# Performance work log

Measured on AMD Instinct MI355X. Metric: run time of the kernel, lower is better.

The kernel has to match this reference:

```python
import jax, jax.numpy as jnp
import numpy as np

C = 256
CQK = C // 8  # 32

def setup_inputs() -> dict:
    key = jax.random.key(0)
    ks = jax.random.split(key, 9)
    B, H, W = 4, 64, 64
    shp = (B, C, H, W)
    v = jax.random.normal(ks[0], shp, dtype=jnp.float32)
    k = jax.random.normal(ks[1], shp, dtype=jnp.float32)
    q = jax.random.normal(ks[2], shp, dtype=jnp.float32)
    s = 1.0 / np.sqrt(C)
    Wq = jax.random.normal(ks[3], (CQK, C), dtype=jnp.float32) * s
    bq = jnp.zeros((CQK,), dtype=jnp.float32)
    Wk = jax.random.normal(ks[4], (CQK, C), dtype=jnp.float32) * s
    bk = jnp.zeros((CQK,), dtype=jnp.float32)
    Wv = jax.random.normal(ks[5], (C, C), dtype=jnp.float32) * s
    bv = jnp.zeros((C,), dtype=jnp.float32)
    # torch inits gamma=0 (out == v); use small nonzero so attention path is exercised
    gamma = jnp.full((1,), 0.5, dtype=jnp.float32)
    return {"v": v, "k": k, "q": q, "Wq": Wq, "bq": bq, "Wk": Wk, "bk": bk,
            "Wv": Wv, "bv": bv, "gamma": gamma}

def reference(v, k, q, Wq, bq, Wk, bk, Wv, bv, gamma):
    B, Cc, Hh, Ww = v.shape
    N = Hh * Ww
    # 1x1 convs == per-pixel channel matmuls
    pq = jnp.einsum('oc,bchw->bohw', Wq, q) + bq[None, :, None, None]  # B,CQK,H,W
    pk = jnp.einsum('oc,bchw->bohw', Wk, k) + bk[None, :, None, None]
    pv = jnp.einsum('oc,bchw->bohw', Wv, v) + bv[None, :, None, None]  # B,C,H,W
    pq = pq.reshape(B, -1, N)  # B,d,N
    pk = pk.reshape(B, -1, N)
    pv = pv.reshape(B, Cc, N)
    # energy[b,n,m] = <q_n, k_m>; softmax over m (keys)
    energy = jnp.einsum('bdn,bdm->bnm', pq, pk)
    attn = jax.nn.softmax(energy, axis=-1)
    # out[b,c,n] = sum_m v[b,c,m] * attn[b,n,m]
    out = jnp.einsum('bcm,bnm->bcn', pv, attn).reshape(B, Cc, Hh, Ww)
    return gamma * out + v
```

## Files before the change

### kernel.cpp

```cpp
#include <hip/hip_runtime.h>
#include <hip/hip_bf16.h>

typedef __attribute__((ext_vector_type(8))) short short8_t;
typedef __attribute__((ext_vector_type(4))) unsigned short ushort4_t;
typedef __attribute__((ext_vector_type(4))) float float4_t;

#define B_   4
#define C_   256
#define N_   4096
#define DQK  32
#define LOG2E 1.4426950408889634f

#define VMCNT4   asm volatile("s_waitcnt vmcnt(4)" ::: "memory")
#define VMCNT0   asm volatile("s_waitcnt vmcnt(0)" ::: "memory")
#define LGKM0    asm volatile("s_waitcnt lgkmcnt(0)" ::: "memory")
#define SBAR     __builtin_amdgcn_s_barrier()
#define SCHEDB   __builtin_amdgcn_sched_barrier(0)

__device__ __forceinline__ unsigned short f2bf(float x) {
    union { float f; unsigned int u; } v; v.f = x;
    unsigned int r = v.u + 0x7FFFu + ((v.u >> 16) & 1u);
    return (unsigned short)(r >> 16);
}
__device__ __forceinline__ unsigned short f2bf_hw(float x) {
    return __bfloat16_as_ushort(__float2bfloat16(x));
}
__device__ __forceinline__ float bf2f(unsigned short u) {
    union { unsigned int u; float f; } v; v.u = ((unsigned int)u) << 16; return v.f;
}

__global__ __launch_bounds__(256) void cast_w_k(
        const float* __restrict__ Wq, const float* __restrict__ Wk,
        const float* __restrict__ Wv,
        unsigned short* __restrict__ Wqb, unsigned short* __restrict__ Wkb,
        unsigned short* __restrict__ Wvb) {
    int i = blockIdx.x * 256 + threadIdx.x;
    if (i < 8192)            Wqb[i] = f2bf(Wq[i]);
    else if (i < 16384)      Wkb[i - 8192] = f2bf(Wk[i - 8192]);
    else                     Wvb[i - 16384] = f2bf(Wv[i - 16384]);
}

__global__ __launch_bounds__(256) void proj_qk_k(
        const float* __restrict__ q_in, const float* __restrict__ k_in,
        const unsigned short* __restrict__ Wqb, const unsigned short* __restrict__ Wkb,
        const float* __restrict__ bq, const float* __restrict__ bk,
        unsigned short* __restrict__ pqT, unsigned short* __restrict__ pkT) {
    int b = blockIdx.y, z = blockIdx.z;
    const float* X = z ? k_in : q_in;
    const unsigned short* W = z ? Wkb : Wqb;
    const float* bias = z ? bk : bq;
    unsigned short* P = z ? pkT : pqT;
    float scl = z ? 1.0f : LOG2E;
    int tid = threadIdx.x, wave = tid >> 6, lane = tid & 63, l15 = lane & 15, g = lane >> 4;
    int nb = blockIdx.x * 64 + wave * 16;
    float4_t acc0 = {0.f, 0.f, 0.f, 0.f}, acc1 = {0.f, 0.f, 0.f, 0.f};
    const float* Xcol = X + (size_t)b * C_ * N_ + nb + l15;
#pragma unroll
    for (int kk = 0; kk < 8; ++kk) {
        short8_t a;
#pragma unroll
        for (int j = 0; j < 8; ++j)
            a[j] = (short)f2bf(Xcol[(size_t)(kk * 32 + 8 * g + j) * N_]);
        short8_t b0 = *(const short8_t*)(W + (size_t)l15 * C_ + kk * 32 + 8 * g);
        short8_t b1 = *(const short8_t*)(W + (size_t)(16 + l15) * C_ + kk * 32 + 8 * g);
        acc0 = __builtin_amdgcn_mfma_f32_16x16x32_bf16(a, b0, acc0, 0, 0, 0);
        acc1 = __builtin_amdgcn_mfma_f32_16x16x32_bf16(a, b1, acc1, 0, 0, 0);
    }
#pragma unroll
    for (int r = 0; r < 4; ++r) {
        int n = nb + 4 * g + r;
        P[((size_t)b * N_ + n) * DQK + l15]      = f2bf((acc0[r] + bias[l15]) * scl);
        P[((size_t)b * N_ + n) * DQK + 16 + l15] = f2bf((acc1[r] + bias[16 + l15]) * scl);
    }
}

__global__ __launch_bounds__(256) void proj_v_k(
        const float* __restrict__ v_in, const unsigned short* __restrict__ Wvb,
        const float* __restrict__ bv, unsigned short* __restrict__ pv) {
    int b = blockIdx.y;
    int tid = threadIdx.x, wave = tid >> 6, lane = tid & 63, l15 = lane & 15, g = lane >> 4;
    int mb = blockIdx.x * 16;
    int m = mb + l15;
    int k32 = m & 31;
    int pcol = (k32 < 16) ? ((k32 >> 2) * 8 + (k32 & 3))
                          : (((k32 - 16) >> 2) * 8 + 4 + (k32 & 3));
    int mcol = (m & ~31) + pcol;
    float4_t acc[4];
#pragma unroll
    for (int i = 0; i < 4; ++i) acc[i] = (float4_t){0.f, 0.f, 0.f, 0.f};
    const float* Vcol = v_in + (size_t)b * C_ * N_ + mb + l15;
#pragma unroll
    for (int kk = 0; kk < 8; ++kk) {
        short8_t bf;
#pragma unroll
        for (int j = 0; j < 8; ++j)
            bf[j] = (short)f2bf(Vcol[(size_t)(kk * 32 + 8 * g + j) * N_]);
#pragma unroll
        for (int ct = 0; ct < 4; ++ct) {
            short8_t af = *(const short8_t*)(Wvb + (size_t)(wave * 64 + ct * 16 + l15) * C_ + kk * 32 + 8 * g);
            acc[ct] = __builtin_amdgcn_mfma_f32_16x16x32_bf16(af, bf, acc[ct], 0, 0, 0);
        }
    }
#pragma unroll
    for (int ct = 0; ct < 4; ++ct)
#pragma unroll
        for (int r = 0; r < 4; ++r) {
            int c = wave * 64 + ct * 16 + 4 * g + r;
            pv[((size_t)b * C_ + c) * N_ + mcol] = f2bf(acc[ct][r] + bv[c]);
        }
}

__global__ __launch_bounds__(512, 4) void attn_split_k(
        const unsigned short* __restrict__ pqT, const unsigned short* __restrict__ pkT,
        const unsigned short* __restrict__ pv,
        unsigned short* __restrict__ accP, float* __restrict__ lP, int KS) {
    __shared__ __align__(16) unsigned short VT[256][64];
    __shared__ __align__(16) short8_t Pl[2][4][2][4][16];
    int nqb = gridDim.x;
    int lin = blockIdx.x + nqb * (blockIdx.y + KS * blockIdx.z);
    int cpx = (nqb * KS * 4) >> 3;
    int sl  = (lin & 7) * cpx + (lin >> 3);
    int qbi = sl % nqb;
    int s   = (sl / nqb) % KS;
    int b   = sl / (nqb * KS);

    int kps = N_ / KS, ks0 = s * kps, nt = kps >> 6;
    int tid = threadIdx.x, wave = tid >> 6, lane = tid & 63, l15 = lane & 15, g = lane >> 4;
    int qb = qbi * 64;
    bool prod = wave < 4;
    int qs = wave & 3;
    int rl = lane >> 3, cl = (lane & 7) ^ rl;
    int sw = (l15 & 7) << 4;

    short8_t qf = *(const short8_t*)(pqT + ((size_t)b * N_ + qb + qs * 16 + l15) * DQK + 8 * g);
    float4_t acc[2][4];
#pragma unroll
    for (int i = 0; i < 2; ++i)
#pragma unroll
        for (int j = 0; j < 4; ++j) acc[i][j] = (float4_t){0.f, 0.f, 0.f, 0.f};
    float l_acc = 0.f;
    const float4_t zero4 = {0.f, 0.f, 0.f, 0.f};
    const char* pvb8 = (const char*)(pv + (size_t)b * C_ * N_);
    const char* pkTb = (const char*)pkT + (size_t)b * N_ * DQK * 2;

    unsigned soff[4];
#pragma unroll
    for (int i = 0; i < 4; ++i)
        soff[i] = (unsigned)(((wave * 32 + i * 8 + rl) * N_ + ks0 + 8 * cl) * 2);
    unsigned koff = (unsigned)(((ks0 + l15) * DQK + 8 * g) * 2);
    const char* vbA = (const char*)&VT[0][0] + (wave * 32 + l15) * 128 + ((16 * g) ^ sw);
    const char* vbB = (const char*)&VT[0][0] + (wave * 32 + l15) * 128 + ((64 + 16 * g) ^ sw);
    char* PlB = (char*)&Pl[0][0][0][0][0];
    const char* prd = PlB + g * 256 + l15 * 16;
    char* pwr = PlB + qs * 2048 + g * 256 + l15 * 16;

    short8_t kf[4];

#define STAGE()                                                               \
    _Pragma("unroll")                                                         \
    for (int i_ = 0; i_ < 4; ++i_) {                                          \
        __builtin_amdgcn_global_load_lds(                                     \
            (const __attribute__((address_space(1))) unsigned int*)(const void*)(pvb8 + soff[i_]), \
            (__attribute__((address_space(3))) unsigned int*)(void*)((char*)&VT[0][0] + (wave * 32 + i_ * 8) * 128), \
            16, 0, 0);                                                        \
        soff[i_] += 128;                                                      \
    }

#define KFLOAD()                                                              \
    _Pragma("unroll")                                                         \
    for (int it_ = 0; it_ < 4; ++it_)                                         \
        kf[it_] = *(const short8_t*)(pkTb + koff + it_ * 1024);               \
    koff += 4096;

#define VREAD(DST)                                                            \
    _Pragma("unroll")                                                         \
    for (int ct_ = 0; ct_ < 2; ++ct_) {                                       \
        DST[ct_][0] = *(const short8_t*)(vbA + ct_ * 2048);                   \
        DST[ct_][1] = *(const short8_t*)(vbB + ct_ * 2048);                   \
    }

#define PFREAD(DST, CBOFF)                                                    \
    _Pragma("unroll")                                                         \
    for (int qt_ = 0; qt_ < 4; ++qt_)                                         \
        _Pragma("unroll")                                                     \
        for (int kh_ = 0; kh_ < 2; ++kh_)                                     \
            DST[qt_][kh_] = *(const short8_t*)(prd + (CBOFF) + qt_ * 2048 + kh_ * 1024);

#define QKWR(NBOFF)                                                           \
    {                                                                          \
        float4_t sv_[4];                                                       \
        _Pragma("unroll")                                                      \
        for (int it_ = 0; it_ < 4; ++it_)                                      \
            sv_[it_] = __builtin_amdgcn_mfma_f32_16x16x32_bf16(kf[it_], qf, zero4, 0, 0, 0); \
        float p_[16];                                                          \
        _Pragma("unroll")                                                      \
        for (int it_ = 0; it_ < 4; ++it_)                                      \
            _Pragma("unroll")                                                  \
            for (int r_ = 0; r_ < 4; ++r_)                                     \
                p_[it_ * 4 + r_] = exp2f(sv_[it_][r_]);                        \
        l_acc += ((p_[0] + p_[1]) + (p_[2] + p_[3])) + ((p_[4] + p_[5]) + (p_[6] + p_[7])) \
               + ((p_[8] + p_[9]) + (p_[10] + p_[11])) + ((p_[12] + p_[13]) + (p_[14] + p_[15])); \
        short8_t pb0_, pb1_;                                                   \
        _Pragma("unroll")                                                      \
        for (int j_ = 0; j_ < 4; ++j_) {                                       \
            pb0_[j_]     = (short)f2bf_hw(p_[j_]);                             \
            pb0_[4 + j_] = (short)f2bf_hw(p_[4 + j_]);                         \
            pb1_[j_]     = (short)f2bf_hw(p_[8 + j_]);                         \
            pb1_[4 + j_] = (short)f2bf_hw(p_[12 + j_]);                        \
        }                                                                      \
        *(short8_t*)(pwr + (NBOFF))        = pb0_;                             \
        *(short8_t*)(pwr + (NBOFF) + 1024) = pb1_;                             \
    }

#define PVM(VF, PF)                                                           \
    _Pragma("unroll")                                                         \
    for (int ct_ = 0; ct_ < 2; ++ct_)                                         \
        _Pragma("unroll")                                                     \
        for (int qt_ = 0; qt_ < 4; ++qt_) {                                   \
            acc[ct_][qt_] = __builtin_amdgcn_mfma_f32_16x16x32_bf16(VF[ct_][0], PF[qt_][0], acc[ct_][qt_], 0, 0, 0); \
            acc[ct_][qt_] = __builtin_amdgcn_mfma_f32_16x16x32_bf16(VF[ct_][1], PF[qt_][1], acc[ct_][qt_], 0, 0, 0); \
        }

#define BODY(T, CBOFF, NBOFF)                                                 \
    {                                                                          \
        if (prod) { VMCNT4; } else { VMCNT0; }                                 \
        SCHEDB;                                                                \
        short8_t vf_[2][2], pf_[4][2];                                         \
        VREAD(vf_)                                                             \
        PFREAD(pf_, CBOFF)                                                     \
        LGKM0; SCHEDB;                                                         \
        if ((T) + 1 < nt) {                                                    \
            STAGE()                                                            \
            SCHEDB;                                                            \
            if (prod) { QKWR(NBOFF) KFLOAD() }                                 \
            SCHEDB;                                                            \
        }                                                                      \
        __builtin_amdgcn_s_setprio(1);                                         \
        PVM(vf_, pf_)                                                          \
        __builtin_amdgcn_s_setprio(0);                                         \
        LGKM0; SCHEDB;                                                         \
        SBAR;                                                                  \
    }

    STAGE()
    if (prod) {
        KFLOAD()
        QKWR(0)
        KFLOAD()
    }
    LGKM0; SCHEDB;
    SBAR;

    for (int t = 0; t < nt; t += 2) {
        BODY(t,     0, 8192)
        BODY(t + 1, 8192, 0)
    }

    if (prod) {
        l_acc += __shfl_xor(l_acc, 16);
        l_acc += __shfl_xor(l_acc, 32);
        if (g == 0)
            lP[(size_t)(b * KS + s) * N_ + qb + qs * 16 + l15] = l_acc;
    }
    unsigned short* accOut = accP + ((size_t)(b * KS + s) * C_) * N_;
#pragma unroll
    for (int ct = 0; ct < 2; ++ct)
#pragma unroll
        for (int qt = 0; qt < 4; ++qt)
#pragma unroll
            for (int r = 0; r < 4; ++r) {
                int c = wave * 32 + ct * 16 + 4 * g + r;
                accOut[(size_t)c * N_ + qb + qt * 16 + l15] = f2bf_hw(acc[ct][qt][r]);
            }
#undef STAGE
#undef KFLOAD
#undef VREAD
#undef PFREAD
#undef QKWR
#undef PVM
#undef BODY
}

__global__ __launch_bounds__(256) void combine_k(
        const unsigned short* __restrict__ accP, const float* __restrict__ lP,
        const float* __restrict__ v_in, const float* __restrict__ gamma,
        float* __restrict__ out, int KS) {
    int i = blockIdx.x * 256 + threadIdx.x;
    const int nq4 = N_ / 4;
    int q0 = (i % nq4) * 4;
    int c  = (i / nq4) % C_;
    int b  = i / (nq4 * C_);
    float4_t num = {0.f, 0.f, 0.f, 0.f}, den = {0.f, 0.f, 0.f, 0.f};
    for (int s = 0; s < KS; ++s) {
        float4_t l4 = *(const float4_t*)(lP + (size_t)(b * KS + s) * N_ + q0);
        ushort4_t a4 = *(const ushort4_t*)(accP + ((size_t)(b * KS + s) * C_ + c) * N_ + q0);
#pragma unroll
        for (int j = 0; j < 4; ++j) {
            den[j] += l4[j];
            num[j] += bf2f(a4[j]);
        }
    }
    float gm = gamma[0];
    size_t idx = ((size_t)(b * C_ + c)) * N_ + q0;
    float4_t vi = *(const float4_t*)(v_in + idx);
    float4_t o;
#pragma unroll
    for (int j = 0; j < 4; ++j) o[j] = gm * num[j] / den[j] + vi[j];
    *(float4_t*)(out + idx) = o;
}

extern "C" void kernel_launch(void* const* d_in, const int* in_sizes, int n_in,
                              void* d_out, int out_size, void* d_ws, size_t ws_size,
                              hipStream_t stream) {
    (void)in_sizes; (void)n_in; (void)out_size;
    const float* v_in  = (const float*)d_in[0];
    const float* k_in  = (const float*)d_in[1];
    const float* q_in  = (const float*)d_in[2];
    const float* Wq    = (const float*)d_in[3];
    const float* bq    = (const float*)d_in[4];
    const float* Wk    = (const float*)d_in[5];
    const float* bk    = (const float*)d_in[6];
    const float* Wv    = (const float*)d_in[7];
    const float* bv    = (const float*)d_in[8];
    const float* gamma = (const float*)d_in[9];
    float* out = (float*)d_out;

    char* ws = (char*)d_ws;
    unsigned short* pvb = (unsigned short*)(ws + 0);
    unsigned short* pqT = (unsigned short*)(ws + 8404992);
    unsigned short* pkT = (unsigned short*)(ws + 9453568);
    unsigned short* Wqb = (unsigned short*)(ws + 10526720);
    unsigned short* Wkb = (unsigned short*)(ws + 10543104);
    unsigned short* Wvb = (unsigned short*)(ws + 10559488);
    const size_t base2 = 10690560;

    int KS = 2;
    while (KS > 1) {
        size_t need = base2 + (size_t)KS * 8388608 + (size_t)KS * 65536;
        if (need <= ws_size) break;
        KS >>= 1;
    }
    unsigned short* accP = (unsigned short*)(ws + base2);
    float* lP = (float*)(ws + base2 + (size_t)KS * 8388608);

    cast_w_k<<<320, 256, 0, stream>>>(Wq, Wk, Wv, Wqb, Wkb, Wvb);
    proj_qk_k<<<dim3(64, 4, 2), 256, 0, stream>>>(q_in, k_in, Wqb, Wkb, bq, bk, pqT, pkT);
    proj_v_k<<<dim3(256, 4), 256, 0, stream>>>(v_in, Wvb, bv, pvb);
    attn_split_k<<<dim3(64, KS, 4), 512, 0, stream>>>(pqT, pkT, pvb, accP, lP, KS);
    combine_k<<<4096, 256, 0, stream>>>(accP, lP, v_in, gamma, out, KS);
}
```

Measured before the change: 94.86 us.

## Double-buffer V tile in LDS to issue next-tile loads before the wait

The V tile staging buffer in shared memory is doubled, so the global-to-LDS load for tile t+1 is issued at the top of each iteration, before waiting on tile t. The vmcnt waits are raised to leave the newly issued loads in flight, which gives the memory latency a full iteration to hide behind the PV MFMAs. The cost is an extra 32 KB of LDS per block, which may reduce how many blocks fit per CU under the launch bound of 4.

Result: slower. 99.34 us (+4.7%).

```diff
diff --git a/kernel.cpp b/kernel.cpp
--- a/kernel.cpp
+++ b/kernel.cpp
@@ -11,6 +11,7 @@
 #define DQK  32
 #define LOG2E 1.4426950408889634f
 
+#define VMCNT8   asm volatile("s_waitcnt vmcnt(8)" ::: "memory")
 #define VMCNT4   asm volatile("s_waitcnt vmcnt(4)" ::: "memory")
 #define VMCNT0   asm volatile("s_waitcnt vmcnt(0)" ::: "memory")
 #define LGKM0    asm volatile("s_waitcnt lgkmcnt(0)" ::: "memory")
@@ -114,7 +115,7 @@
         const unsigned short* __restrict__ pqT, const unsigned short* __restrict__ pkT,
         const unsigned short* __restrict__ pv,
         unsigned short* __restrict__ accP, float* __restrict__ lP, int KS) {
-    __shared__ __align__(16) unsigned short VT[256][64];
+    __shared__ __align__(16) unsigned short VT[2][256][64];
     __shared__ __align__(16) short8_t Pl[2][4][2][4][16];
     int nqb = gridDim.x;
     int lin = blockIdx.x + nqb * (blockIdx.y + KS * blockIdx.z);
@@ -148,20 +149,20 @@
     for (int i = 0; i < 4; ++i)
         soff[i] = (unsigned)(((wave * 32 + i * 8 + rl) * N_ + ks0 + 8 * cl) * 2);
     unsigned koff = (unsigned)(((ks0 + l15) * DQK + 8 * g) * 2);
-    const char* vbA = (const char*)&VT[0][0] + (wave * 32 + l15) * 128 + ((16 * g) ^ sw);
-    const char* vbB = (const char*)&VT[0][0] + (wave * 32 + l15) * 128 + ((64 + 16 * g) ^ sw);
+    const char* vbA = (const char*)&VT[0][0][0] + (wave * 32 + l15) * 128 + ((16 * g) ^ sw);
+    const char* vbB = (const char*)&VT[0][0][0] + (wave * 32 + l15) * 128 + ((64 + 16 * g) ^ sw);
     char* PlB = (char*)&Pl[0][0][0][0][0];
     const char* prd = PlB + g * 256 + l15 * 16;
     char* pwr = PlB + qs * 2048 + g * 256 + l15 * 16;
 
     short8_t kf[4];
 
-#define STAGE()                                                               \
+#define STAGE(RBUF)                                                           \
     _Pragma("unroll")                                                         \
     for (int i_ = 0; i_ < 4; ++i_) {                                          \
         __builtin_amdgcn_global_load_lds(                                     \
             (const __attribute__((address_space(1))) unsigned int*)(const void*)(pvb8 + soff[i_]), \
-            (__attribute__((address_space(3))) unsigned int*)(void*)((char*)&VT[0][0] + (wave * 32 + i_ * 8) * 128), \
+            (__attribute__((address_space(3))) unsigned int*)(void*)((char*)&VT[RBUF][0][0] + (wave * 32 + i_ * 8) * 128), \
             16, 0, 0);                                                        \
         soff[i_] += 128;                                                      \
     }
@@ -172,11 +173,11 @@
         kf[it_] = *(const short8_t*)(pkTb + koff + it_ * 1024);               \
     koff += 4096;
 
-#define VREAD(DST)                                                            \
+#define VREAD(DST, RB)                                                        \
     _Pragma("unroll")                                                         \
     for (int ct_ = 0; ct_ < 2; ++ct_) {                                       \
-        DST[ct_][0] = *(const short8_t*)(vbA + ct_ * 2048);                   \
-        DST[ct_][1] = *(const short8_t*)(vbB + ct_ * 2048);                   \
+        DST[ct_][0] = *(const short8_t*)(vbA + (RB) * 32768 + ct_ * 2048);    \
+        DST[ct_][1] = *(const short8_t*)(vbB + (RB) * 32768 + ct_ * 2048);    \
     }
 
 #define PFREAD(DST, CBOFF)                                                    \
@@ -221,17 +222,21 @@
             acc[ct_][qt_] = __builtin_amdgcn_mfma_f32_16x16x32_bf16(VF[ct_][1], PF[qt_][1], acc[ct_][qt_], 0, 0, 0); \
         }
 
-#define BODY(T, CBOFF, NBOFF)                                                 \
+#define BODY(T, CBOFF, NBOFF, RB)                                             \
     {                                                                          \
-        if (prod) { VMCNT4; } else { VMCNT0; }                                 \
+        if ((T) + 1 < nt) {                                                    \
+            STAGE((RB) ^ 1)                                                    \
+            SCHEDB;                                                            \
+            if (prod) { VMCNT8; } else { VMCNT4; }                             \
+        } else {                                                               \
+            if (prod) { VMCNT4; } else { VMCNT0; }                             \
+        }                                                                      \
         SCHEDB;                                                                \
         short8_t vf_[2][2], pf_[4][2];                                         \
-        VREAD(vf_)                                                             \
+        VREAD(vf_, RB)                                                         \
         PFREAD(pf_, CBOFF)                                                     \
         LGKM0; SCHEDB;                                                         \
         if ((T) + 1 < nt) {                                                    \
-            STAGE()                                                            \
-            SCHEDB;                                                            \
             if (prod) { QKWR(NBOFF) KFLOAD() }                                 \
             SCHEDB;                                                            \
         }                                                                      \
@@ -242,7 +247,7 @@
         SBAR;                                                                  \
     }
 
-    STAGE()
+    STAGE(0)
     if (prod) {
         KFLOAD()
         QKWR(0)
@@ -252,8 +257,8 @@
     SBAR;
 
     for (int t = 0; t < nt; t += 2) {
-        BODY(t,     0, 8192)
-        BODY(t + 1, 8192, 0)
+        BODY(t,     0, 8192, 0)
+        BODY(t + 1, 8192, 0, 1)
     }
 
     if (prod) {
```
